# Kernel optimization log

Measured on AMD Instinct MI355X. Metric: run time of the kernel, lower is better.

Reference implementation:

```python
import jax, jax.numpy as jnp
import numpy as np

K = 1024      # num_embeddings
D = 256       # embedding_dim
BETA = 0.25


def setup_inputs() -> dict:
    key = jax.random.key(0)
    k1, k2 = jax.random.split(key)
    latents = jax.random.normal(k1, (32, D, 32, 32), dtype=jnp.float32)
    # nn.Embedding weight init: uniform(-1/K, 1/K)
    weight = jax.random.uniform(k2, (K, D), dtype=jnp.float32,
                                minval=-1.0 / K, maxval=1.0 / K)
    return {"latents": latents, "weight": weight}


def reference(latents, weight):
    # NCHW -> NHWC
    lat = jnp.transpose(latents, (0, 2, 3, 1))          # [B,H,W,D]
    lat_shape = lat.shape
    flat = lat.reshape(-1, D)                           # [N,D]

    dist = (jnp.sum(flat ** 2, axis=1, keepdims=True)
            - 2.0 * jnp.matmul(flat, weight.T)
            + jnp.sum(weight ** 2, axis=1))             # [N,K]

    min_ind = jnp.argmin(dist, axis=1)                  # [N]
    min_embed = jax.nn.one_hot(min_ind, K, dtype=flat.dtype)  # [N,K]

    # one-hot @ weight == direct gather
    z_q = jnp.take(weight, min_ind, axis=0).reshape(lat_shape)  # [B,H,W,D]

    sg = jax.lax.stop_gradient
    loss = (jnp.mean((sg(z_q) - lat) ** 2)
            + BETA * jnp.mean((z_q - sg(lat)) ** 2))

    # straight-through estimator
    z_q_st = lat + sg(z_q - lat)

    e_mean = jnp.mean(min_embed, axis=0)                # [K]
    perplexity = jnp.exp(-jnp.sum(e_mean * jnp.log(e_mean + 1e-10)))

    z_q_out = jnp.transpose(z_q_st, (0, 3, 1, 2))       # NHWC -> NCHW
    return (loss, z_q_out, perplexity, min_embed, min_ind[:, None])
```

## Files before the change

### kernel.cpp

```cpp
#include <hip/hip_runtime.h>

#define KN 1024
#define DD 256
#define NTOT 32768
#define HW 1024

#define OFF_LOSS 0
#define OFF_ZQ   1
#define OFF_PERP 8388609
#define OFF_EMB  8388610
#define OFF_IND  41943042

#define WS_WSUM2_OFF 4112
#define WS_WBH_OFF   8208
#define WS_WBL_OFF   (8208 + 524288)

#define XS_STRIDE 260
#define THR 3.0e-4f

typedef __bf16 bf16x8 __attribute__((ext_vector_type(8)));
typedef float  f32x4  __attribute__((ext_vector_type(4)));
typedef unsigned short ushort_t;

#define SM_XS    0
#define SM_XFH   33280
#define SM_XFL   49664
#define SM_WSC   66048
#define SM_PART  70144
#define SM_REDV  70144
#define SM_ROWM  71168
#define SM_CCNT  71296
#define SM_CLIST 71424
#define SM_FV    72448
#define SM_ASUM  73472
#define SM_BI    73600
#define SM_LRED  73728
#define SM_SIZE  73760

__device__ __forceinline__ unsigned short bf16_rne(float f) {
    unsigned u = __float_as_uint(f);
    return (unsigned short)((u + 0x7FFFu + ((u >> 16) & 1u)) >> 16);
}

__device__ __forceinline__ float exact_dist(const float* xs, const float* wsC,
                                            const float* asum,
                                            const float* __restrict__ w,
                                            int r, int k) {
    float a = 0.f;
    const float4* wr = (const float4*)(w + k * DD);
    const float4* xr = (const float4*)(xs + r * XS_STRIDE);
    #pragma unroll 4
    for (int q = 0; q < 64; ++q) {
        const float4 wv = wr[q];
        const float4 xv = xr[q];
        a = fmaf(xv.x, wv.x, a);
        a = fmaf(xv.y, wv.y, a);
        a = fmaf(xv.z, wv.z, a);
        a = fmaf(xv.w, wv.w, a);
    }
    return (asum[r] - 2.0f * a) + wsC[k];
}

__global__ __launch_bounds__(256) void vq_prep(const float* __restrict__ w,
                                               float* __restrict__ wsum2,
                                               ushort_t* __restrict__ wBh,
                                               ushort_t* __restrict__ wBl) {
    const int k = blockIdx.x;
    const int d = threadIdx.x;
    float v = w[k * DD + d];
    {
        const int c = k >> 4, s0 = d >> 5, g = (d >> 3) & 3, j = d & 7;
        const int lane = (k & 15) | (g << 4);
        const int idx = (((c * 8 + s0) * 64 + lane) << 3) + j;
        const unsigned short hh = bf16_rne(v);
        wBh[idx] = hh;
        wBl[idx] = bf16_rne(v - __uint_as_float((unsigned)hh << 16));
    }
    float s = v * v;
    #pragma unroll
    for (int off = 32; off; off >>= 1) s += __shfl_down(s, off, 64);
    __shared__ float wsum[4];
    const int wave = d >> 6, lane = d & 63;
    if (lane == 0) wsum[wave] = s;
    __syncthreads();
    if (d == 0) wsum2[k] = (wsum[0] + wsum[1]) + (wsum[2] + wsum[3]);
}

__global__ __launch_bounds__(512, 2) void vq_main(const float* __restrict__ lat,
                                                  const float* __restrict__ w,
                                                  const float* __restrict__ wsum2,
                                                  const ushort_t* __restrict__ wBh,
                                                  const ushort_t* __restrict__ wBl,
                                                  float* __restrict__ out,
                                                  unsigned* __restrict__ cnt,
                                                  double* __restrict__ lossSum) {
    extern __shared__ char smem[];
    float*    xs    = (float*)(smem + SM_XS);
    ushort_t* xfH   = (ushort_t*)(smem + SM_XFH);
    ushort_t* xfL   = (ushort_t*)(smem + SM_XFL);
    float*    wsC   = (float*)(smem + SM_WSC);
    float*    part  = (float*)(smem + SM_PART);
    float*    redv  = (float*)(smem + SM_REDV);
    float*    rowm  = (float*)(smem + SM_ROWM);
    unsigned* ccnt  = (unsigned*)(smem + SM_CCNT);
    int*      clist = (int*)(smem + SM_CLIST);
    float*    fv    = (float*)(smem + SM_FV);
    float*    asum  = (float*)(smem + SM_ASUM);
    int*      bi    = (int*)(smem + SM_BI);
    double*   lred  = (double*)(smem + SM_LRED);

    const int n0  = blockIdx.x * 32;
    const int b   = n0 >> 10;
    const int hw0 = n0 & 1023;
    const int tid = threadIdx.x;
    const int l   = tid & 63;
    const int wv  = tid >> 6;

    {
        const float* base = lat + (size_t)b * (DD * HW) + hw0;
        const int rr = tid & 31, dl = tid >> 5;
        #pragma unroll
        for (int it = 0; it < 16; ++it) {
            const int d = it * 16 + dl;
            xs[rr * XS_STRIDE + d] = base[d * HW + rr];
        }
        for (int i = tid; i < KN; i += 512) wsC[i] = wsum2[i];
    }
    __syncthreads();

    #pragma unroll
    for (int h = 0; h < 2; ++h) {
        if (tid < 256) {
            const int r = tid & 15, seg = tid >> 4;
            float p = 0.f;
            #pragma unroll
            for (int i = 0; i < 16; ++i) {
                float x = xs[(h * 16 + r) * XS_STRIDE + seg * 16 + i];
                p += x * x;
            }
            part[seg * 17 + r] = p;
        }
        __syncthreads();
        if (tid < 16) {
            float a = 0.f;
            #pragma unroll
            for (int s = 0; s < 16; ++s) a += part[s * 17 + tid];
            asum[h * 16 + tid] = a;
        }
        __syncthreads();
    }

    #pragma unroll
    for (int i = 0; i < 2; ++i) {
        const int u  = tid + i * 512;
        const int rt = u >> 9, s0 = (u >> 6) & 7, ll = u & 63;
        const int row = rt * 16 + (ll & 15);
        const int d0  = s0 * 32 + (ll >> 4) * 8;
        const float4 x0 = *(const float4*)(xs + row * XS_STRIDE + d0);
        const float4 x1 = *(const float4*)(xs + row * XS_STRIDE + d0 + 4);
        float xv[8] = {x0.x, x0.y, x0.z, x0.w, x1.x, x1.y, x1.z, x1.w};
        unsigned hh[8], lo[8];
        #pragma unroll
        for (int j = 0; j < 8; ++j) {
            hh[j] = bf16_rne(xv[j]);
            lo[j] = bf16_rne(xv[j] - __uint_as_float(hh[j] << 16));
        }
        uint4 ph, pl;
        ph.x = hh[0] | (hh[1] << 16); ph.y = hh[2] | (hh[3] << 16);
        ph.z = hh[4] | (hh[5] << 16); ph.w = hh[6] | (hh[7] << 16);
        pl.x = lo[0] | (lo[1] << 16); pl.y = lo[2] | (lo[3] << 16);
        pl.z = lo[4] | (lo[5] << 16); pl.w = lo[6] | (lo[7] << 16);
        *(uint4*)(xfH + u * 8) = ph;
        *(uint4*)(xfL + u * 8) = pl;
    }
    __syncthreads();

    f32x4 acc[2][8];
    #pragma unroll
    for (int rt = 0; rt < 2; ++rt)
        #pragma unroll
        for (int c = 0; c < 8; ++c)
            acc[rt][c] = (f32x4){0.f, 0.f, 0.f, 0.f};

    {
        bf16x8 ah0, ah1, al0, al1;
        bf16x8 pbh0, pbl0, pbh1, pbl1;

        #define BOFF(s0_, c_) (((size_t)(((wv * 8 + (c_)) * 8 + (s0_)) * 64 + l)) * 8)
        pbh0 = *(const bf16x8*)(wBh + BOFF(0, 0));
        pbl0 = *(const bf16x8*)(wBl + BOFF(0, 0));
        pbh1 = *(const bf16x8*)(wBh + BOFF(0, 1));
        pbl1 = *(const bf16x8*)(wBl + BOFF(0, 1));

        #pragma unroll
        for (int it = 0; it < 64; ++it) {
            const int s0 = it >> 3, c = it & 7;
            if (c == 0) {
                ah0 = *(const bf16x8*)(xfH + ((0 * 8 + s0) * 64 + l) * 8);
                ah1 = *(const bf16x8*)(xfH + ((1 * 8 + s0) * 64 + l) * 8);
                al0 = *(const bf16x8*)(xfL + ((0 * 8 + s0) * 64 + l) * 8);
                al1 = *(const bf16x8*)(xfL + ((1 * 8 + s0) * 64 + l) * 8);
            }
            bf16x8 bh, bl;
            if ((it & 1) == 0) { bh = pbh0; bl = pbl0; } else { bh = pbh1; bl = pbl1; }
            if (it + 2 < 64) {
                const int nit = it + 2, ns = nit >> 3, nc = nit & 7;
                if ((it & 1) == 0) {
                    pbh0 = *(const bf16x8*)(wBh + BOFF(ns, nc));
                    pbl0 = *(const bf16x8*)(wBl + BOFF(ns, nc));
                } else {
                    pbh1 = *(const bf16x8*)(wBh + BOFF(ns, nc));
                    pbl1 = *(const bf16x8*)(wBl + BOFF(ns, nc));
                }
            }
            acc[0][c] = __builtin_amdgcn_mfma_f32_16x16x32_bf16(ah0, bh, acc[0][c], 0, 0, 0);
            acc[1][c] = __builtin_amdgcn_mfma_f32_16x16x32_bf16(ah1, bh, acc[1][c], 0, 0, 0);
            acc[0][c] = __builtin_amdgcn_mfma_f32_16x16x32_bf16(ah0, bl, acc[0][c], 0, 0, 0);
            acc[1][c] = __builtin_amdgcn_mfma_f32_16x16x32_bf16(ah1, bl, acc[1][c], 0, 0, 0);
            acc[0][c] = __builtin_amdgcn_mfma_f32_16x16x32_bf16(al0, bh, acc[0][c], 0, 0, 0);
            acc[1][c] = __builtin_amdgcn_mfma_f32_16x16x32_bf16(al1, bh, acc[1][c], 0, 0, 0);
        }
        #undef BOFF
    }

    float rmv[2][4];
    #pragma unroll
    for (int rt = 0; rt < 2; ++rt)
        #pragma unroll
        for (int q = 0; q < 4; ++q) rmv[rt][q] = 3.4e38f;
    #pragma unroll
    for (int c = 0; c < 8; ++c) {
        const float cv = wsC[(wv * 8 + c) * 16 + (l & 15)];
        #pragma unroll
        for (int rt = 0; rt < 2; ++rt) {
            #pragma unroll
            for (int q = 0; q < 4; ++q) {
                const float dv = fmaf(-2.0f, acc[rt][c][q], cv);
                acc[rt][c][q] = dv;
                rmv[rt][q] = fminf(rmv[rt][q], dv);
            }
        }
    }
    #pragma unroll
    for (int rt = 0; rt < 2; ++rt)
        #pragma unroll
        for (int q = 0; q < 4; ++q) {
            float m = rmv[rt][q];
            #pragma unroll
            for (int off = 1; off < 16; off <<= 1) m = fminf(m, __shfl_xor(m, off, 64));
            rmv[rt][q] = m;
        }
    if ((l & 15) == 0) {
        const int g = l >> 4;
        #pragma unroll
        for (int rt = 0; rt < 2; ++rt)
            #pragma unroll
            for (int q = 0; q < 4; ++q)
                redv[wv * 32 + rt * 16 + g * 4 + q] = rmv[rt][q];
    }
    __syncthreads();
    if (tid < 32) {
        float m = redv[tid];
        #pragma unroll
        for (int ww = 1; ww < 8; ++ww) m = fminf(m, redv[ww * 32 + tid]);
        rowm[tid] = m;
        ccnt[tid] = 0u;
    }
    __syncthreads();

    #pragma unroll
    for (int rt = 0; rt < 2; ++rt) {
        #pragma unroll
        for (int q = 0; q < 4; ++q) {
            const int row = rt * 16 + ((l >> 4) << 2) + q;
            const float lim = rowm[row] + THR;
            #pragma unroll
            for (int c = 0; c < 8; ++c) {
                if (acc[rt][c][q] <= lim) {
                    const unsigned pos = atomicAdd(&ccnt[row], 1u);
                    if (pos < 8) clist[row * 8 + pos] = (wv * 8 + c) * 16 + (l & 15);
                }
            }
        }
    }
    __syncthreads();

    if (tid < 256) {
        const int r = tid >> 3, ci = tid & 7;
        const unsigned cc = ccnt[r];
        if (cc >= 2u) {
            if (cc <= 8u) {
                if ((unsigned)ci < cc)
                    fv[r * 8 + ci] = exact_dist(xs, wsC, asum, w, r, clist[r * 8 + ci]);
            } else if (ci == 0) {
                float bvv = 3.4e38f; int bkk = 0;
                for (int k = 0; k < KN; ++k) {
                    const float dvv = exact_dist(xs, wsC, asum, w, r, k);
                    if (dvv < bvv) { bvv = dvv; bkk = k; }
                }
                bi[r] = bkk;
            }
        }
    }
    __syncthreads();
    if (tid < 32) {
        const unsigned cc = ccnt[tid];
        int kk;
        if (cc == 1u) kk = clist[tid * 8];
        else if (cc <= 8u) {
            float v = fv[tid * 8]; kk = clist[tid * 8];
            for (unsigned ci = 1; ci < cc; ++ci) {
                const float ov = fv[tid * 8 + ci];
                const int   ok = clist[tid * 8 + ci];
                if (ov < v || (ov == v && ok < kk)) { v = ov; kk = ok; }
            }
        } else kk = bi[tid];
        bi[tid] = kk;
        out[OFF_IND + n0 + tid] = (float)kk;
        atomicAdd(&cnt[kk], 1u);
    }
    __syncthreads();

    {
        float2* emb2 = reinterpret_cast<float2*>(out + OFF_EMB) + (size_t)n0 * (KN / 2);
        #pragma unroll
        for (int it = 0; it < 32; ++it) {
            const int f = it * 512 + tid;
            const int r = f >> 9;
            const int kq = (f & 511) * 2;
            const int tt = bi[r];
            float2 v2;
            v2.x = (kq     == tt) ? 1.0f : 0.0f;
            v2.y = (kq + 1 == tt) ? 1.0f : 0.0f;
            emb2[f] = v2;
        }
    }

    #pragma unroll
    for (int h = 0; h < 2; ++h) {
        if (tid < 256) {
            const int n0h = n0 + h * 16;
            const int bb = n0h >> 10, hw0h = n0h & 1023;
            float* zq_out = out + OFF_ZQ + (size_t)bb * (DD * HW) + hw0h;
            const int jj = tid & 15, db = tid >> 4;
            const int krow = bi[h * 16 + jj];
            float lsum = 0.f;
            #pragma unroll
            for (int it = 0; it < 16; ++it) {
                const int d = it * 16 + db;
                const float latv = xs[(h * 16 + jj) * XS_STRIDE + d];
                const float zq   = w[krow * DD + d];
                const float dif  = zq - latv;
                zq_out[d * HW + jj] = latv + dif;
                lsum = fmaf(dif, dif, lsum);
            }
            float s2 = lsum;
            #pragma unroll
            for (int off = 32; off; off >>= 1) s2 += __shfl_down(s2, off, 64);
            if ((tid & 63) == 0) lred[wv] = (double)s2;
        }
        __syncthreads();
        if (tid == 0) {
            double t = (lred[0] + lred[1]) + (lred[2] + lred[3]);
            atomicAdd(lossSum, t);
        }
        __syncthreads();
    }
}

__global__ __launch_bounds__(1024) void vq_finalize(const unsigned* __restrict__ cnt,
                                                    const double* __restrict__ lossSum,
                                                    float* __restrict__ out) {
    const int t = threadIdx.x;
    __shared__ float red[16];
    const float e = (float)cnt[t] * (1.0f / 32768.0f);
    float s = e * logf(e + 1e-10f);
    #pragma unroll
    for (int off = 32; off; off >>= 1) s += __shfl_down(s, off, 64);
    const int wave = t >> 6, lane = t & 63;
    if (lane == 0) red[wave] = s;
    __syncthreads();
    if (t == 0) {
        float tot = 0.f;
        #pragma unroll
        for (int i = 0; i < 16; ++i) tot += red[i];
        out[OFF_PERP] = expf(-tot);
        const float m = (float)(lossSum[0] * (1.0 / 8388608.0));
        out[OFF_LOSS] = m + 0.25f * m;
    }
}

extern "C" void kernel_launch(void* const* d_in, const int* in_sizes, int n_in,
                              void* d_out, int out_size, void* d_ws, size_t ws_size,
                              hipStream_t stream) {
    const float* lat = (const float*)d_in[0];
    const float* w   = (const float*)d_in[1];

    char* ws = (char*)d_ws;
    double*   lossSum = (double*)ws;
    unsigned* cnt     = (unsigned*)(ws + 8);
    float*    wsum2   = (float*)(ws + WS_WSUM2_OFF);
    ushort_t* wBh     = (ushort_t*)(ws + WS_WBH_OFF);
    ushort_t* wBl     = (ushort_t*)(ws + WS_WBL_OFF);
    float*    out     = (float*)d_out;

    hipMemsetAsync(d_ws, 0, 4104, stream);

    hipFuncSetAttribute(reinterpret_cast<const void*>(vq_main),
                        hipFuncAttributeMaxDynamicSharedMemorySize, SM_SIZE);

    vq_prep<<<KN, 256, 0, stream>>>(w, wsum2, wBh, wBl);
    vq_main<<<NTOT / 32, 512, SM_SIZE, stream>>>(lat, w, wsum2, wBh, wBl, out, cnt, lossSum);
    vq_finalize<<<1, 1024, 0, stream>>>(cnt, lossSum, out);
}
```

Baseline: 131.0 us.

## Vectorize latent loads and zq stores, add nontemporal stores, parallelize fallback search

Loads the latent tile with 128-bit nontemporal loads and writes z_q using all 512 threads with paired float2 nontemporal stores, moving that write out of the loss loop. The one-hot and index outputs also switch to nontemporal stores. The full-codebook fallback search is split across 8 threads per row, and the launch bound is raised to request 4 blocks per CU, which may force register spills. Shared memory offsets shift slightly.

```diff
diff --git a/kernel.cpp b/kernel.cpp
--- a/kernel.cpp
+++ b/kernel.cpp
@@ -20,6 +20,7 @@
 
 typedef __bf16 bf16x8 __attribute__((ext_vector_type(8)));
 typedef float  f32x4  __attribute__((ext_vector_type(4)));
+typedef float  f32x2  __attribute__((ext_vector_type(2)));
 typedef unsigned short ushort_t;
 
 #define SM_XS    0
@@ -28,14 +29,14 @@
 #define SM_WSC   66048
 #define SM_PART  70144
 #define SM_REDV  70144
-#define SM_ROWM  71168
-#define SM_CCNT  71296
-#define SM_CLIST 71424
-#define SM_FV    72448
-#define SM_ASUM  73472
-#define SM_BI    73600
-#define SM_LRED  73728
-#define SM_SIZE  73760
+#define SM_ROWM  71232
+#define SM_CCNT  71360
+#define SM_CLIST 71488
+#define SM_FV    72512
+#define SM_ASUM  73536
+#define SM_BI    73664
+#define SM_LRED  73792
+#define SM_SIZE  73824
 
 __device__ __forceinline__ unsigned short bf16_rne(float f) {
     unsigned u = __float_as_uint(f);
@@ -86,7 +87,7 @@
     if (d == 0) wsum2[k] = (wsum[0] + wsum[1]) + (wsum[2] + wsum[3]);
 }
 
-__global__ __launch_bounds__(512, 2) void vq_main(const float* __restrict__ lat,
+__global__ __launch_bounds__(512, 4) void vq_main(const float* __restrict__ lat,
                                                   const float* __restrict__ w,
                                                   const float* __restrict__ wsum2,
                                                   const ushort_t* __restrict__ wBh,
@@ -118,13 +119,19 @@
 
     {
         const float* base = lat + (size_t)b * (DD * HW) + hw0;
-        const int rr = tid & 31, dl = tid >> 5;
-        #pragma unroll
-        for (int it = 0; it < 16; ++it) {
-            const int d = it * 16 + dl;
-            xs[rr * XS_STRIDE + d] = base[d * HW + rr];
-        }
-        for (int i = tid; i < KN; i += 512) wsC[i] = wsum2[i];
+        #pragma unroll
+        for (int it = 0; it < 4; ++it) {
+            const int u = it * 512 + tid;
+            const int d = u >> 3, r4 = (u & 7) * 4;
+            const f32x4 v = __builtin_nontemporal_load(
+                reinterpret_cast<const f32x4*>(base + d * HW + r4));
+            xs[(r4 + 0) * XS_STRIDE + d] = v.x;
+            xs[(r4 + 1) * XS_STRIDE + d] = v.y;
+            xs[(r4 + 2) * XS_STRIDE + d] = v.z;
+            xs[(r4 + 3) * XS_STRIDE + d] = v.w;
+        }
+        wsC[tid] = wsum2[tid];
+        wsC[tid + 512] = wsum2[tid + 512];
     }
     __syncthreads();
 
@@ -292,13 +299,14 @@
             if (cc <= 8u) {
                 if ((unsigned)ci < cc)
                     fv[r * 8 + ci] = exact_dist(xs, wsC, asum, w, r, clist[r * 8 + ci]);
-            } else if (ci == 0) {
-                float bvv = 3.4e38f; int bkk = 0;
-                for (int k = 0; k < KN; ++k) {
+            } else {
+                float bvv = 3.4e38f; int bkk = ci * 128;
+                for (int k = ci * 128; k < ci * 128 + 128; ++k) {
                     const float dvv = exact_dist(xs, wsC, asum, w, r, k);
                     if (dvv < bvv) { bvv = dvv; bkk = k; }
                 }
-                bi[r] = bkk;
+                fv[r * 8 + ci] = bvv;
+                clist[r * 8 + ci] = bkk;
             }
         }
     }
@@ -307,41 +315,56 @@
         const unsigned cc = ccnt[tid];
         int kk;
         if (cc == 1u) kk = clist[tid * 8];
-        else if (cc <= 8u) {
+        else {
+            const unsigned ncand = (cc <= 8u) ? cc : 8u;
             float v = fv[tid * 8]; kk = clist[tid * 8];
-            for (unsigned ci = 1; ci < cc; ++ci) {
+            for (unsigned ci = 1; ci < ncand; ++ci) {
                 const float ov = fv[tid * 8 + ci];
                 const int   ok = clist[tid * 8 + ci];
                 if (ov < v || (ov == v && ok < kk)) { v = ov; kk = ok; }
             }
-        } else kk = bi[tid];
+        }
         bi[tid] = kk;
-        out[OFF_IND + n0 + tid] = (float)kk;
+        __builtin_nontemporal_store((float)kk, &out[OFF_IND + n0 + tid]);
         atomicAdd(&cnt[kk], 1u);
     }
     __syncthreads();
 
     {
-        float2* emb2 = reinterpret_cast<float2*>(out + OFF_EMB) + (size_t)n0 * (KN / 2);
+        float* zq_out = out + OFF_ZQ + (size_t)b * (DD * HW) + hw0;
+        #pragma unroll
+        for (int it = 0; it < 8; ++it) {
+            const int u = it * 512 + tid;
+            const int d = u >> 4, j2 = (u & 15) * 2;
+            const float la0 = xs[(j2 + 0) * XS_STRIDE + d];
+            const float la1 = xs[(j2 + 1) * XS_STRIDE + d];
+            const float z0  = w[bi[j2 + 0] * DD + d];
+            const float z1  = w[bi[j2 + 1] * DD + d];
+            f32x2 v;
+            v.x = la0 + (z0 - la0);
+            v.y = la1 + (z1 - la1);
+            __builtin_nontemporal_store(v, reinterpret_cast<f32x2*>(zq_out + d * HW + j2));
+        }
+    }
+
+    {
+        f32x2* emb2 = reinterpret_cast<f32x2*>(out + OFF_EMB) + (size_t)n0 * (KN / 2);
         #pragma unroll
         for (int it = 0; it < 32; ++it) {
             const int f = it * 512 + tid;
             const int r = f >> 9;
             const int kq = (f & 511) * 2;
             const int tt = bi[r];
-            float2 v2;
+            f32x2 v2;
             v2.x = (kq     == tt) ? 1.0f : 0.0f;
             v2.y = (kq + 1 == tt) ? 1.0f : 0.0f;
-            emb2[f] = v2;
+            __builtin_nontemporal_store(v2, &emb2[f]);
         }
     }
 
     #pragma unroll
     for (int h = 0; h < 2; ++h) {
         if (tid < 256) {
-            const int n0h = n0 + h * 16;
-            const int bb = n0h >> 10, hw0h = n0h & 1023;
-            float* zq_out = out + OFF_ZQ + (size_t)bb * (DD * HW) + hw0h;
             const int jj = tid & 15, db = tid >> 4;
             const int krow = bi[h * 16 + jj];
             float lsum = 0.f;
@@ -351,7 +374,6 @@
                 const float latv = xs[(h * 16 + jj) * XS_STRIDE + d];
                 const float zq   = w[krow * DD + d];
                 const float dif  = zq - latv;
-                zq_out[d * HW + jj] = latv + dif;
                 lsum = fmaf(dif, dif, lsum);
             }
             float s2 = lsum;
@@ -404,10 +426,10 @@
     ushort_t* wBl     = (ushort_t*)(ws + WS_WBL_OFF);
     float*    out     = (float*)d_out;
 
-    hipMemsetAsync(d_ws, 0, 4104, stream);
-
-    hipFuncSetAttribute(reinterpret_cast<const void*>(vq_main),
-                        hipFuncAttributeMaxDynamicSharedMemorySize, SM_SIZE);
+    (void)hipMemsetAsync(d_ws, 0, 4104, stream);
+
+    (void)hipFuncSetAttribute(reinterpret_cast<const void*>(vq_main),
+                              hipFuncAttributeMaxDynamicSharedMemorySize, SM_SIZE);
 
     vq_prep<<<KN, 256, 0, stream>>>(w, wsum2, wBh, wBl);
     vq_main<<<NTOT / 32, 512, SM_SIZE, stream>>>(lat, w, wsum2, wBh, wBl, out, cnt, lossSum);
```

Measured after the change: 129.6 us (median of 3 runs). Within noise of the previous version (-1.1%).
